# Performance work log

Measured on AMD Instinct MI355X. Metric: run time of the kernel, lower is better.

Reference implementation:

```python
import jax, jax.numpy as jnp
import numpy as np

B, H, W, C, F = 8, 128, 128, 256, 256

def setup_inputs() -> dict:
    key = jax.random.key(0)
    k1, k2, k3 = jax.random.split(key, 3)
    x = jax.random.normal(k1, (B, H, W, C), dtype=jnp.float32)
    style = jax.random.normal(k2, (B, 1, 1, C), dtype=jnp.float32)
    # he_uniform over fan_in = 3*3*C
    limit = np.sqrt(6.0 / (3 * 3 * C)).astype(np.float32)
    kernel = jax.random.uniform(k3, (3, 3, C, F), dtype=jnp.float32, minval=-limit, maxval=limit)
    return {"x": x, "style": style, "kernel": kernel}

def reference(x, style, kernel):
    b, h, w_, c = x.shape
    f = kernel.shape[-1]
    # per-sample modulation: [B,1,1,C,1] * [1,3,3,C,F] -> [B,3,3,C,F]
    wmod = kernel[None] * (style[..., None] + 1.0)
    demod = jnp.sqrt(jnp.sum(jnp.square(wmod), axis=(1, 2, 3), keepdims=True) + 1e-8)
    wmod = wmod / demod
    # grouped conv trick: x -> [1, B*C, H, W], filters -> [3,3,C,B*F], groups=B
    xg = jnp.transpose(x, (0, 3, 1, 2)).reshape(1, b * c, h, w_)
    wf = jnp.transpose(wmod, (1, 2, 3, 0, 4)).reshape(3, 3, c, b * f)
    y = jax.lax.conv_general_dilated(
        xg, wf, window_strides=(1, 1), padding='SAME',
        dimension_numbers=('NCHW', 'HWIO', 'NCHW'),
        feature_group_count=b)
    y = y.reshape(b, f, h, w_)
    return jnp.transpose(y, (0, 2, 3, 1))
```

## Files before the change

### kernel.cpp

```cpp
#include <hip/hip_runtime.h>
#include <hip/hip_bf16.h>


#define NB 8
#define NH 128
#define NW 128
#define NC 256
#define NF 256

typedef __attribute__((ext_vector_type(8))) short bf16x8;
typedef __attribute__((ext_vector_type(4))) float f32x4;

__global__ void k_cvt(const float* __restrict__ x, ushort* __restrict__ xbf) {
    int i = (blockIdx.x * blockDim.x + threadIdx.x) * 4;
    float4 v = *(const float4*)(x + i);
    union { ushort4 u; __hip_bfloat16 h[4]; } o;
    o.h[0] = __float2bfloat16(v.x);
    o.h[1] = __float2bfloat16(v.y);
    o.h[2] = __float2bfloat16(v.z);
    o.h[3] = __float2bfloat16(v.w);
    *(ushort4*)(xbf + i) = o.u;
}

__global__ void k_modw(const float* __restrict__ kern, const float* __restrict__ style,
                       ushort* __restrict__ wm) {
    int b = blockIdx.x >> 8;
    int f = blockIdx.x & 255;
    int c = threadIdx.x;
    float s = style[b * 256 + c] + 1.0f;
    float w[9];
    float acc = 0.f;
#pragma unroll
    for (int t = 0; t < 9; ++t) {
        w[t] = kern[(t * 256 + c) * 256 + f] * s;
        acc += w[t] * w[t];
    }
#pragma unroll
    for (int off = 32; off; off >>= 1) acc += __shfl_down(acc, off);
    __shared__ float part[4];
    if ((threadIdx.x & 63) == 0) part[threadIdx.x >> 6] = acc;
    __syncthreads();
    float total = part[0] + part[1] + part[2] + part[3];
    float inv = 1.0f / sqrtf(total + 1e-8f);
#pragma unroll
    for (int t = 0; t < 9; ++t) {
        union { ushort u; __hip_bfloat16 h; } o;
        o.h = __float2bfloat16(w[t] * inv);
        wm[(((b * 9 + t) * 256 + f) * 256) + c] = o.u;
    }
}

__global__ void __launch_bounds__(256)
k_conv(const ushort* __restrict__ xbf, const ushort* __restrict__ wm,
       float* __restrict__ out) {
    const int bidx = blockIdx.x;
    const int fh = bidx & 1;
    const int h  = (bidx >> 1) & 127;
    const int b  = bidx >> 8;

    __shared__ ushort As[3][130 * 32];
    __shared__ ushort Bs[128 * 32];

    const int tid = threadIdx.x;
    const int wave = tid >> 6, lane = tid & 63;
    const int wm_ = wave & 1, wn_ = wave >> 1;
    const int lrow = lane & 15;
    const int quad = lane >> 4;

    for (int i = tid; i < 3 * 2 * 32; i += 256) {
        int dh = i >> 6;
        int side = (i >> 5) & 1;
        int cc = i & 31;
        As[dh][(side ? 129 : 0) * 32 + cc] = 0;
    }
#pragma unroll
    for (int dh = 0; dh < 3; ++dh) {
        int hp = h + dh - 1;
        if (hp < 0 || hp >= 128) {
            for (int i = tid; i < 130 * 32; i += 256) As[dh][i] = 0;
        }
    }

    f32x4 acc[4][4];
    const f32x4 zero4 = {0.f, 0.f, 0.f, 0.f};
#pragma unroll
    for (int mi = 0; mi < 4; ++mi)
#pragma unroll
        for (int ni = 0; ni < 4; ++ni) acc[mi][ni] = zero4;

    const int wload = tid >> 2;
    const int cload = (tid & 3) * 8;

    for (int c0 = 0; c0 < 256; c0 += 32) {
        __syncthreads();
#pragma unroll
        for (int dh = 0; dh < 3; ++dh) {
            int hp = h + dh - 1;
            if (hp >= 0 && hp < 128) {
                const ushort* src = xbf + ((b * 128 + hp) * 128) * 256 + c0;
#pragma unroll
                for (int j = 0; j < 2; ++j) {
                    int w = j * 64 + wload;
                    uint4 v = *(const uint4*)(src + w * 256 + cload);
                    *(uint4*)&As[dh][(w + 1) * 32 + cload] = v;
                }
            }
        }
#pragma unroll
        for (int dh = 0; dh < 3; ++dh) {
#pragma unroll
            for (int dw = 0; dw < 3; ++dw) {
                const int tap = dh * 3 + dw;
                __syncthreads();
                {
                    const ushort* src = wm + ((b * 9 + tap) * 256 + fh * 128) * 256 + c0;
#pragma unroll
                    for (int j = 0; j < 2; ++j) {
                        int fl = j * 64 + wload;
                        uint4 v = *(const uint4*)(src + fl * 256 + cload);
                        *(uint4*)&Bs[fl * 32 + cload] = v;
                    }
                }
                __syncthreads();
                bf16x8 af[4], bfr[4];
#pragma unroll
                for (int ni = 0; ni < 4; ++ni) {
                    int fl = wn_ * 64 + ni * 16 + lrow;
                    bfr[ni] = *(const bf16x8*)&Bs[fl * 32 + quad * 8];
                }
#pragma unroll
                for (int mi = 0; mi < 4; ++mi) {
                    int w = wm_ * 64 + mi * 16 + lrow;
                    af[mi] = *(const bf16x8*)&As[dh][(w + dw) * 32 + quad * 8];
                }
#pragma unroll
                for (int mi = 0; mi < 4; ++mi)
#pragma unroll
                    for (int ni = 0; ni < 4; ++ni)
                        acc[mi][ni] = __builtin_amdgcn_mfma_f32_16x16x32_bf16(
                            af[mi], bfr[ni], acc[mi][ni], 0, 0, 0);
            }
        }
    }

    float* obase = out + ((b * 128 + h) * 128) * 256 + fh * 128;
#pragma unroll
    for (int mi = 0; mi < 4; ++mi) {
        int wrow = wm_ * 64 + mi * 16 + quad * 4;
#pragma unroll
        for (int ni = 0; ni < 4; ++ni) {
            int f = wn_ * 64 + ni * 16 + lrow;
            f32x4 v = acc[mi][ni];
#pragma unroll
            for (int r = 0; r < 4; ++r) {
                obase[(wrow + r) * 256 + f] = v[r];
            }
        }
    }
}

extern "C" void kernel_launch(void* const* d_in, const int* in_sizes, int n_in,
                              void* d_out, int out_size, void* d_ws, size_t ws_size,
                              hipStream_t stream) {
    const float* x     = (const float*)d_in[0];
    const float* style = (const float*)d_in[1];
    const float* kern  = (const float*)d_in[2];
    float* out = (float*)d_out;

    ushort* xbf = (ushort*)d_ws;
    ushort* wmod = xbf + (size_t)NB * NH * NW * NC;

    k_cvt<<<(NB * NH * NW * NC) / (256 * 4), 256, 0, stream>>>(x, xbf);
    k_modw<<<NB * NF, 256, 0, stream>>>(kern, style, wmod);
    k_conv<<<NB * NH * 2, 256, 0, stream>>>(xbf, wmod, out);
}
```

Baseline: 405.9 us.

## Use direct global-to-LDS loads with double-buffered weight tiles in conv

The conv kernel now fills shared memory with global_load_lds, so data no longer passes through registers. Weight tiles are double-buffered so the next tap's load overlaps the MFMA work on the current tap, which cuts the barriers from two per tap to one. The LDS layout changes to a channel-chunk-major form with padding to reduce bank conflicts, and the block index is remapped so batch varies fastest. The convert kernel also handles eight elements per thread. The cost is more LDS use and a subtle dependence on the ordering of async loads against the single barrier.

```diff
diff --git a/kernel.cpp b/kernel.cpp
--- a/kernel.cpp
+++ b/kernel.cpp
@@ -11,15 +11,35 @@
 typedef __attribute__((ext_vector_type(8))) short bf16x8;
 typedef __attribute__((ext_vector_type(4))) float f32x4;
 
+#define PA 2080
+#define A_ROW (4 * PA)
+#define A_BYTES (3 * A_ROW)
+#define B_BUF (4 * PA)
+#define LDS_BYTES (A_BYTES + 2 * B_BUF)
+
+__device__ __forceinline__ ushort f2bf(float v) {
+    union { ushort u; __hip_bfloat16 h; } o;
+    o.h = __float2bfloat16(v);
+    return o.u;
+}
+
+__device__ __forceinline__ void gload16(const ushort* g, const char* l) {
+    __builtin_amdgcn_global_load_lds(
+        (const __attribute__((address_space(1))) void*)g,
+        (__attribute__((address_space(3))) void*)l,
+        16, 0, 0);
+}
+
 __global__ void k_cvt(const float* __restrict__ x, ushort* __restrict__ xbf) {
-    int i = (blockIdx.x * blockDim.x + threadIdx.x) * 4;
-    float4 v = *(const float4*)(x + i);
-    union { ushort4 u; __hip_bfloat16 h[4]; } o;
-    o.h[0] = __float2bfloat16(v.x);
-    o.h[1] = __float2bfloat16(v.y);
-    o.h[2] = __float2bfloat16(v.z);
-    o.h[3] = __float2bfloat16(v.w);
-    *(ushort4*)(xbf + i) = o.u;
+    size_t i = ((size_t)blockIdx.x * 256 + threadIdx.x) * 8;
+    float4 a = *(const float4*)(x + i);
+    float4 b = *(const float4*)(x + i + 4);
+    union { ushort s[8]; uint4 u; } o;
+    o.s[0] = f2bf(a.x); o.s[1] = f2bf(a.y);
+    o.s[2] = f2bf(a.z); o.s[3] = f2bf(a.w);
+    o.s[4] = f2bf(b.x); o.s[5] = f2bf(b.y);
+    o.s[6] = f2bf(b.z); o.s[7] = f2bf(b.w);
+    *(uint4*)(xbf + i) = o.u;
 }
 
 __global__ void k_modw(const float* __restrict__ kern, const float* __restrict__ style,
@@ -44,9 +64,7 @@
     float inv = 1.0f / sqrtf(total + 1e-8f);
 #pragma unroll
     for (int t = 0; t < 9; ++t) {
-        union { ushort u; __hip_bfloat16 h; } o;
-        o.h = __float2bfloat16(w[t] * inv);
-        wm[(((b * 9 + t) * 256 + f) * 256) + c] = o.u;
+        wm[(((b * 9 + t) * 256 + f) * 256) + c] = f2bf(w[t] * inv);
     }
 }
 
@@ -54,12 +72,14 @@
 k_conv(const ushort* __restrict__ xbf, const ushort* __restrict__ wm,
        float* __restrict__ out) {
     const int bidx = blockIdx.x;
-    const int fh = bidx & 1;
-    const int h  = (bidx >> 1) & 127;
-    const int b  = bidx >> 8;
-
-    __shared__ ushort As[3][130 * 32];
-    __shared__ ushort Bs[128 * 32];
+    const int b    = bidx & 7;
+    const int rest = bidx >> 3;
+    const int fh   = rest & 1;
+    const int h    = rest >> 1;
+
+    __shared__ __align__(16) char smem[LDS_BYTES];
+    char* As = smem;
+    char* Bs = smem + A_BYTES;
 
     const int tid = threadIdx.x;
     const int wave = tid >> 6, lane = tid & 63;
@@ -67,19 +87,11 @@
     const int lrow = lane & 15;
     const int quad = lane >> 4;
 
-    for (int i = tid; i < 3 * 2 * 32; i += 256) {
-        int dh = i >> 6;
-        int side = (i >> 5) & 1;
-        int cc = i & 31;
-        As[dh][(side ? 129 : 0) * 32 + cc] = 0;
-    }
-#pragma unroll
-    for (int dh = 0; dh < 3; ++dh) {
-        int hp = h + dh - 1;
-        if (hp < 0 || hp >= 128) {
-            for (int i = tid; i < 130 * 32; i += 256) As[dh][i] = 0;
-        }
-    }
+    {
+        const uint4 z = {0, 0, 0, 0};
+        for (int i = tid; i < A_BYTES / 16; i += 256) ((uint4*)As)[i] = z;
+    }
+    __syncthreads();
 
     f32x4 acc[4][4];
     const f32x4 zero4 = {0.f, 0.f, 0.f, 0.f};
@@ -88,62 +100,74 @@
 #pragma unroll
         for (int ni = 0; ni < 4; ++ni) acc[mi][ni] = zero4;
 
-    const int wload = tid >> 2;
-    const int cload = (tid & 3) * 8;
+    const ushort* xb_base = xbf + (size_t)b * 128 * 128 * 256;
+    const ushort* wm_base = wm + ((size_t)b * 9) * 256 * 256 + (size_t)fh * 128 * 256;
 
     for (int c0 = 0; c0 < 256; c0 += 32) {
-        __syncthreads();
-#pragma unroll
-        for (int dh = 0; dh < 3; ++dh) {
+#pragma unroll
+        for (int i = 0; i < 6; ++i) {
+            int L = wave * 6 + i;
+            int dh = L >> 3, rem = L & 7;
+            int p = rem >> 1, half = rem & 1;
             int hp = h + dh - 1;
             if (hp >= 0 && hp < 128) {
-                const ushort* src = xbf + ((b * 128 + hp) * 128) * 256 + c0;
-#pragma unroll
-                for (int j = 0; j < 2; ++j) {
-                    int w = j * 64 + wload;
-                    uint4 v = *(const uint4*)(src + w * 256 + cload);
-                    *(uint4*)&As[dh][(w + 1) * 32 + cload] = v;
+                int w = half * 64 + lane;
+                const ushort* g = xb_base + ((size_t)hp * 128 + w) * 256 + c0 + p * 8;
+                const char* l = As + dh * A_ROW + p * PA + 16 + half * 1024;
+                gload16(g, l);
+            }
+        }
+        {
+#pragma unroll
+            for (int i = 0; i < 2; ++i) {
+                int s = wave * 2 + i;
+                int p = s >> 1, halfp = s & 1;
+                int f = halfp * 64 + lane;
+                const ushort* g = wm_base + ((size_t)(0 * 256) + f) * 256 + c0 + p * 8;
+                const char* l = Bs + p * PA + halfp * 1024;
+                gload16(g, l);
+            }
+        }
+        __syncthreads();
+
+#pragma unroll
+        for (int tap = 0; tap < 9; ++tap) {
+            const int dh = tap / 3, dw = tap % 3;
+            const int cur = tap & 1;
+            if (tap < 8) {
+                int nxt = (tap + 1) & 1;
+#pragma unroll
+                for (int i = 0; i < 2; ++i) {
+                    int s = wave * 2 + i;
+                    int p = s >> 1, halfp = s & 1;
+                    int f = halfp * 64 + lane;
+                    const ushort* g = wm_base + ((size_t)((tap + 1) * 256) + f) * 256 + c0 + p * 8;
+                    const char* l = Bs + nxt * B_BUF + p * PA + halfp * 1024;
+                    gload16(g, l);
                 }
             }
-        }
-#pragma unroll
-        for (int dh = 0; dh < 3; ++dh) {
-#pragma unroll
-            for (int dw = 0; dw < 3; ++dw) {
-                const int tap = dh * 3 + dw;
-                __syncthreads();
-                {
-                    const ushort* src = wm + ((b * 9 + tap) * 256 + fh * 128) * 256 + c0;
-#pragma unroll
-                    for (int j = 0; j < 2; ++j) {
-                        int fl = j * 64 + wload;
-                        uint4 v = *(const uint4*)(src + fl * 256 + cload);
-                        *(uint4*)&Bs[fl * 32 + cload] = v;
-                    }
-                }
-                __syncthreads();
-                bf16x8 af[4], bfr[4];
-#pragma unroll
-                for (int ni = 0; ni < 4; ++ni) {
-                    int fl = wn_ * 64 + ni * 16 + lrow;
-                    bfr[ni] = *(const bf16x8*)&Bs[fl * 32 + quad * 8];
-                }
-#pragma unroll
-                for (int mi = 0; mi < 4; ++mi) {
-                    int w = wm_ * 64 + mi * 16 + lrow;
-                    af[mi] = *(const bf16x8*)&As[dh][(w + dw) * 32 + quad * 8];
-                }
-#pragma unroll
-                for (int mi = 0; mi < 4; ++mi)
-#pragma unroll
-                    for (int ni = 0; ni < 4; ++ni)
-                        acc[mi][ni] = __builtin_amdgcn_mfma_f32_16x16x32_bf16(
-                            af[mi], bfr[ni], acc[mi][ni], 0, 0, 0);
-            }
-        }
-    }
-
-    float* obase = out + ((b * 128 + h) * 128) * 256 + fh * 128;
+            bf16x8 af[4], bfr[4];
+#pragma unroll
+            for (int ni = 0; ni < 4; ++ni) {
+                int f = wn_ * 64 + ni * 16 + lrow;
+                bfr[ni] = *(const bf16x8*)(Bs + cur * B_BUF + quad * PA + f * 16);
+            }
+#pragma unroll
+            for (int mi = 0; mi < 4; ++mi) {
+                int s = wm_ * 64 + mi * 16 + lrow + dw;
+                af[mi] = *(const bf16x8*)(As + dh * A_ROW + quad * PA + s * 16);
+            }
+#pragma unroll
+            for (int mi = 0; mi < 4; ++mi)
+#pragma unroll
+                for (int ni = 0; ni < 4; ++ni)
+                    acc[mi][ni] = __builtin_amdgcn_mfma_f32_16x16x32_bf16(
+                        af[mi], bfr[ni], acc[mi][ni], 0, 0, 0);
+            __syncthreads();
+        }
+    }
+
+    float* obase = out + (((size_t)b * 128 + h) * 128) * 256 + fh * 128;
 #pragma unroll
     for (int mi = 0; mi < 4; ++mi) {
         int wrow = wm_ * 64 + mi * 16 + quad * 4;
@@ -153,7 +177,7 @@
             f32x4 v = acc[mi][ni];
 #pragma unroll
             for (int r = 0; r < 4; ++r) {
-                obase[(wrow + r) * 256 + f] = v[r];
+                obase[(size_t)(wrow + r) * 256 + f] = v[r];
             }
         }
     }
@@ -167,10 +191,10 @@
     const float* kern  = (const float*)d_in[2];
     float* out = (float*)d_out;
 
-    ushort* xbf = (ushort*)d_ws;
+    ushort* xbf  = (ushort*)d_ws;
     ushort* wmod = xbf + (size_t)NB * NH * NW * NC;
 
-    k_cvt<<<(NB * NH * NW * NC) / (256 * 4), 256, 0, stream>>>(x, xbf);
+    k_cvt<<<(NB * NH * NW * NC) / (256 * 8), 256, 0, stream>>>(x, xbf);
     k_modw<<<NB * NF, 256, 0, stream>>>(kern, style, wmod);
     k_conv<<<NB * NH * 2, 256, 0, stream>>>(xbf, wmod, out);
 }
```

Measured after the change: 436.9 us. 1.08x slower.
